# Optimization experiments

Hardware: AMD Instinct MI355X
Metric: run time of the kernel (lower is better)

Reference implementation:

```python
import jax, jax.numpy as jnp
import numpy as np

WIN = 8   # window size
NH = 6    # num heads
DIM = 192
PDIM = 256
S = 32    # D=H=W spatial extent


def window_partition(x, w):
    # x: (B, D, H, W, C) -> (nW, w**3, C)
    B, D, H, Wd, C = x.shape
    x = x.reshape(B, D // w, w, H // w, w, Wd // w, w, C)
    x = x.transpose(0, 1, 3, 5, 2, 4, 6, 7)
    return x.reshape(-1, w * w * w, C)


def window_reverse(win, w, B, D, H, Wd):
    C = win.shape[-1]
    x = win.reshape(B, D // w, H // w, Wd // w, w, w, w, C)
    x = x.transpose(0, 1, 4, 2, 5, 3, 6, 7)
    return x.reshape(B, D, H, Wd, C)


def layernorm(x, g, b, eps=1e-5):
    m = x.mean(-1, keepdims=True)
    v = ((x - m) ** 2).mean(-1, keepdims=True)
    return (x - m) / jnp.sqrt(v + eps) * g + b


def setup_inputs() -> dict:
    key = jax.random.key(0)
    ks = jax.random.split(key, 8)
    return {
        "x": jax.random.normal(ks[0], (1, DIM, S, S, S), jnp.float32),
        "prev_x": jax.random.normal(ks[1], (1, PDIM, S, S, S), jnp.float32),
        "fc1_w": jax.random.normal(ks[2], (PDIM, PDIM), jnp.float32) * 0.02,
        "fc1_b": jnp.zeros((PDIM,), jnp.float32),
        "fc2_w": jax.random.normal(ks[3], (DIM, PDIM), jnp.float32) * 0.02,
        "fc2_b": jnp.zeros((DIM,), jnp.float32),
        "q_w": jax.random.normal(ks[4], (DIM, DIM), jnp.float32) * 0.02,
        "q_b": jnp.zeros((DIM,), jnp.float32),
        "kv_w": jax.random.normal(ks[5], (2 * DIM, DIM), jnp.float32) * 0.02,
        "v_b": jnp.zeros((DIM,), jnp.float32),
        "proj_w": jax.random.normal(ks[6], (DIM, DIM), jnp.float32) * 0.02,
        "proj_b": jnp.zeros((DIM,), jnp.float32),
        "logit_scale": jnp.log(10.0) * jnp.ones((NH, 1, 1), jnp.float32),
        "ln_g": jnp.ones((DIM,), jnp.float32),
        "ln_b": jnp.zeros((DIM,), jnp.float32),
    }


def reference(x, prev_x, fc1_w, fc1_b, fc2_w, fc2_b, q_w, q_b, kv_w, v_b,
              proj_w, proj_b, logit_scale, ln_g, ln_b):
    B, C, D, H, Wd = x.shape
    xc = x.transpose(0, 2, 3, 4, 1)       # (B, D, H, W, C)
    pc = prev_x.transpose(0, 2, 3, 4, 1)   # (B, D, H, W, prev_dim)
    # mlp_match: Linear -> GELU(exact) -> Linear
    pc = jax.nn.gelu(pc @ fc1_w.T + fc1_b, approximate=False) @ fc2_w.T + fc2_b
    xw = window_partition(xc, WIN)         # (nW, N, C)
    pw = window_partition(pc, WIN)         # (nW, N, C)
    nW, N, _ = xw.shape
    hd = C // NH
    # q from x1, kv from x2 (k has no bias, v does)
    q = (xw @ q_w.T + q_b).reshape(nW, N, NH, hd).transpose(0, 2, 1, 3)
    kv_bias = jnp.concatenate([jnp.zeros_like(v_b), v_b])
    kv = (pw @ kv_w.T + kv_bias).reshape(nW, N, 2, NH, hd).transpose(2, 0, 3, 1, 4)
    k_, v_ = kv[0], kv[1]                  # (nW, H, N, hd)
    # cosine attention with clamped learned logit scale
    qn = q / jnp.maximum(jnp.linalg.norm(q, axis=-1, keepdims=True), 1e-12)
    kn = k_ / jnp.maximum(jnp.linalg.norm(k_, axis=-1, keepdims=True), 1e-12)
    scale = jnp.exp(jnp.minimum(logit_scale, jnp.log(1.0 / 0.01)))  # (H,1,1)
    attn = jnp.einsum('whnd,whmd->whnm', qn, kn) * scale
    attn = jax.nn.softmax(attn, axis=-1)
    out = jnp.einsum('whnm,whmd->whnd', attn, v_).transpose(0, 2, 1, 3).reshape(nW, N, C)
    out = out @ proj_w.T + proj_b
    xw = xw + layernorm(out, ln_g, ln_b)   # residual + cross_norm
    xr = window_reverse(xw, WIN, B, D, H, Wd)
    return xr.transpose(0, 4, 1, 2, 3)     # back to (B, C, D, H, W)
```

## Files before the change

### kernel.cpp

```cpp
#include <hip/hip_runtime.h>
#include <stdint.h>

typedef unsigned short u16;
typedef unsigned int u32;
typedef short short8 __attribute__((ext_vector_type(8)));
typedef float f32x4 __attribute__((ext_vector_type(4)));
typedef u32 u32x4 __attribute__((ext_vector_type(4)));

#define T_TOT 32768

__device__ __forceinline__ u16 f2bf(float f) {
  u32 u = __float_as_uint(f);
  return (u16)((u + 0x7fffu + ((u >> 16) & 1u)) >> 16);
}
__device__ __forceinline__ float bf2f(u16 h) {
  return __uint_as_float(((u32)h) << 16);
}
__device__ __forceinline__ u32 pk2(float a, float b) {
  return (u32)f2bf(a) | ((u32)f2bf(b) << 16);
}
__device__ __forceinline__ u32 cvtpk(float a, float b) {
  u32 r;
  asm("v_cvt_pk_bf16_f32 %0, %1, %2" : "=v"(r) : "v"(a), "v"(b));
  return r;
}

__device__ __forceinline__ void gld_lds16(const void* g, void* l) {
  __builtin_amdgcn_global_load_lds(
      (const __attribute__((address_space(1))) u32*)g,
      (__attribute__((address_space(3))) u32*)l, 16, 0, 0);
}

__device__ __forceinline__ void plswap(u32& a, u32& b) {
#if __has_builtin(__builtin_amdgcn_permlane32_swap) && \
    __has_builtin(__builtin_amdgcn_permlane16_swap)
  typedef u32 u32x2v __attribute__((ext_vector_type(2)));
  u32x2v r = __builtin_amdgcn_permlane32_swap(a, b, false, false);
  u32x2v w = __builtin_amdgcn_permlane16_swap(r[0], r[1], false, false);
  a = w[0]; b = w[1];
#else
  asm volatile(
      "s_nop 2\n\t"
      "v_permlane32_swap_b32 %0, %1\n\t"
      "s_nop 2\n\t"
      "v_permlane16_swap_b32 %0, %1\n\t"
      "s_nop 2"
      : "+v"(a), "+v"(b));
#endif
}

__global__ __launch_bounds__(256) void k_wconv(
    const float* __restrict__ fc1, const float* __restrict__ fc2,
    const float* __restrict__ qw, const float* __restrict__ kvw,
    const float* __restrict__ pw, u16* __restrict__ out) {
  int idx = blockIdx.x * 256 + threadIdx.x;
  const float* src; int K; int rel; u16* dst;
  if (idx < 8192)       { src = fc1; K = 256; rel = idx;         dst = out; }
  else if (idx < 14336) { src = fc2; K = 256; rel = idx - 8192;  dst = out + 65536; }
  else if (idx < 18944) { src = qw;  K = 192; rel = idx - 14336; dst = out + 114688; }
  else if (idx < 28160) { src = kvw; K = 192; rel = idx - 18944; dst = out + 151552; }
  else                  { src = pw;  K = 192; rel = idx - 28160; dst = out + 225280; }
  int nch = K >> 3;
  int m = rel / nch, ch = rel % nch;
  const float* sp = src + (size_t)m * K + ch * 8;
  int pos = (ch & ~7) | ((ch ^ m) & 7);
  u16* dp = dst + (size_t)m * K + pos * 8;
  ushort4 u0, u1;
  u0.x = f2bf(sp[0]); u0.y = f2bf(sp[1]); u0.z = f2bf(sp[2]); u0.w = f2bf(sp[3]);
  u1.x = f2bf(sp[4]); u1.y = f2bf(sp[5]); u1.z = f2bf(sp[6]); u1.w = f2bf(sp[7]);
  *(ushort4*)(dp) = u0;
  *(ushort4*)(dp + 4) = u1;
}

template<int C>
__global__ __launch_bounds__(256) void k_transpose(const float* __restrict__ src,
                                                   u16* __restrict__ dst) {
  __shared__ u16 sT[64][72];
  int c0 = blockIdx.x * 64, t0 = blockIdx.y * 64;
  int tid = threadIdx.x;
  for (int i = tid; i < 1024; i += 256) {
    int row = i >> 4;
    int tb  = (i & 15) * 4;
    const float* sp = src + (size_t)(c0 + row) * T_TOT + t0 + tb;
    float4 v = *(const float4*)sp;
    ushort4 u;
    u.x = f2bf(v.x); u.y = f2bf(v.y); u.z = f2bf(v.z); u.w = f2bf(v.w);
    *(ushort4*)(&sT[row][tb]) = u;
  }
  __syncthreads();
  int tl = tid & 63;
  int jb = tid >> 6;
  for (int p = 0; p < 2; ++p) {
    int j = jb + 4 * p;
    int t = t0 + tl;
    u16 e[8];
#pragma unroll
    for (int e8 = 0; e8 < 8; ++e8) e[e8] = sT[j * 8 + e8][tl];
    int pos = (c0 >> 3) + (j ^ (t & 7));
    uint4 o;
    o.x = (u32)e[0] | ((u32)e[1] << 16);
    o.y = (u32)e[2] | ((u32)e[3] << 16);
    o.z = (u32)e[4] | ((u32)e[5] << 16);
    o.w = (u32)e[6] | ((u32)e[7] << 16);
    *(uint4*)(dst + (size_t)t * C + pos * 8) = o;
  }
}

enum { EPI_FC1 = 0, EPI_FC2 = 1, EPI_Q = 2, EPI_KV = 3 };

template<int M, int K, int EPI>
__global__ __launch_bounds__(256) void k_gemm(const u16* __restrict__ W,
    const u16* __restrict__ B, const float* __restrict__ bias,
    const float* __restrict__ ls,
    u16* __restrict__ out, u16* __restrict__ out2) {
  __shared__ u16 lW[64 * 64];
  __shared__ u16 lB[128 * 64];
  int tid = threadIdx.x;
  int lane = tid & 63, wid = tid >> 6;
  int g = lane >> 4, c = lane & 15;
  int wm = wid >> 1, wt = wid & 1;
  int t0 = blockIdx.x * 128, m0 = blockIdx.y * 64;
  f32x4 acc[2][4];
#pragma unroll
  for (int i = 0; i < 2; ++i)
#pragma unroll
    for (int j = 0; j < 4; ++j) acc[i][j] = f32x4{0.f, 0.f, 0.f, 0.f};

  for (int s = 0; s < K / 64; ++s) {
    __syncthreads();
#pragma unroll
    for (int i0 = 0; i0 < 512; i0 += 256) {
      int i = i0 + tid;
      int r = i >> 3, ch = i & 7;
      gld_lds16(W + (size_t)(m0 + r) * K + s * 64 + ch * 8,
                lW + (size_t)(i & ~63) * 8);
    }
#pragma unroll
    for (int i0 = 0; i0 < 1024; i0 += 256) {
      int i = i0 + tid;
      int r = i >> 3, ch = i & 7;
      gld_lds16(B + (size_t)(t0 + r) * K + s * 64 + ch * 8,
                lB + (size_t)(i & ~63) * 8);
    }
    __syncthreads();
#pragma unroll
    for (int kc = 0; kc < 2; ++kc) {
      short8 af[2], bfr[4];
#pragma unroll
      for (int mt = 0; mt < 2; ++mt) {
        int r = wm * 32 + mt * 16 + c;
        af[mt] = *(const short8*)(lW + r * 64 + (((kc * 4 + g) ^ (r & 7)) << 3));
      }
#pragma unroll
      for (int tt = 0; tt < 4; ++tt) {
        int r = wt * 64 + tt * 16 + c;
        bfr[tt] = *(const short8*)(lB + r * 64 + (((kc * 4 + g) ^ (r & 7)) << 3));
      }
#pragma unroll
      for (int mt = 0; mt < 2; ++mt)
#pragma unroll
        for (int tt = 0; tt < 4; ++tt)
          acc[mt][tt] = __builtin_amdgcn_mfma_f32_16x16x32_bf16(
              af[mt], bfr[tt], acc[mt][tt], 0, 0, 0);
    }
  }

  float vv[2][4][4];
#pragma unroll
  for (int mt = 0; mt < 2; ++mt) {
    int m_base = m0 + wm * 32 + mt * 16 + 4 * g;
    float br[4];
    if constexpr (EPI == EPI_KV) {
      if (m_base < 192) { br[0] = br[1] = br[2] = br[3] = 0.f; }
      else {
        float4 b4 = *(const float4*)(bias + (m_base - 192));
        br[0] = b4.x; br[1] = b4.y; br[2] = b4.z; br[3] = b4.w;
      }
    } else {
      float4 b4 = *(const float4*)(bias + m_base);
      br[0] = b4.x; br[1] = b4.y; br[2] = b4.z; br[3] = b4.w;
    }
#pragma unroll
    for (int tt = 0; tt < 4; ++tt)
#pragma unroll
      for (int r = 0; r < 4; ++r) vv[mt][tt][r] = acc[mt][tt][r] + br[r];
  }

  if constexpr (EPI == EPI_Q || EPI == EPI_KV) {
    if (EPI == EPI_Q || m0 < 192) {
      float sc = 1.0f;
      if constexpr (EPI == EPI_Q) {
        int headq = (m0 + wm * 32) >> 5;
        sc = __expf(fminf(ls[headq], 4.6051701859880914f)) * 1.4426950408889634f;
      }
#pragma unroll
      for (int tt = 0; tt < 4; ++tt) {
        float ss = 0.f;
#pragma unroll
        for (int mt = 0; mt < 2; ++mt)
#pragma unroll
          for (int r = 0; r < 4; ++r) ss += vv[mt][tt][r] * vv[mt][tt][r];
        ss += __shfl_xor(ss, 16);
        ss += __shfl_xor(ss, 32);
        float rn = sc / fmaxf(sqrtf(ss), 1e-12f);
#pragma unroll
        for (int mt = 0; mt < 2; ++mt)
#pragma unroll
          for (int r = 0; r < 4; ++r) vv[mt][tt][r] *= rn;
      }
    }
  }

#pragma unroll
  for (int mt = 0; mt < 2; ++mt) {
    int m_base = m0 + wm * 32 + mt * 16 + 4 * g;
#pragma unroll
    for (int tt = 0; tt < 4; ++tt) {
      int t = t0 + wt * 64 + tt * 16 + c;
      float v[4];
#pragma unroll
      for (int r = 0; r < 4; ++r) v[r] = vv[mt][tt][r];
      if constexpr (EPI == EPI_FC1) {
#pragma unroll
        for (int r = 0; r < 4; ++r)
          v[r] = 0.5f * v[r] * (1.0f + erff(v[r] * 0.70710678118654752f));
      }
      if constexpr (EPI == EPI_FC1 || EPI == EPI_FC2) {
        ushort4 u;
        u.x = f2bf(v[0]); u.y = f2bf(v[1]); u.z = f2bf(v[2]); u.w = f2bf(v[3]);
        int pos = (m_base >> 3) ^ (t & 7);
        *(ushort4*)(out + (size_t)t * M + (pos << 3) + (m_base & 7)) = u;
      } else {
        int z = t >> 10, y = (t >> 5) & 31, xx = t & 31;
        int win = ((z >> 3) << 4) + ((y >> 3) << 2) + (xx >> 3);
        int n = ((z & 7) << 6) + ((y & 7) << 3) + (xx & 7);
        if (EPI == EPI_Q) {
          int head = m_base >> 5, dim = m_base & 31;
          ushort4 u;
          u.x = f2bf(v[0]); u.y = f2bf(v[1]); u.z = f2bf(v[2]); u.w = f2bf(v[3]);
          *(ushort4*)(out + ((size_t)(win * 6 + head) * 512 + n) * 32 + dim) = u;
        } else if (m_base < 192) {
          int head = m_base >> 5, dim = m_base & 31;
          ushort4 u;
          u.x = f2bf(v[0]); u.y = f2bf(v[1]); u.z = f2bf(v[2]); u.w = f2bf(v[3]);
          *(ushort4*)(out + ((size_t)(win * 6 + head) * 512 + n) * 36 + dim) = u;
        } else {
          int vb = m_base - 192;
          int head = vb >> 5, dimb = vb & 31;
#pragma unroll
          for (int r = 0; r < 4; ++r) {
            int dimr = dimb + r;
            out2[((size_t)(win * 6 + head) * 32 + dimr) * 512 +
                 (((n >> 3) ^ (dimr & 7)) << 3) + (n & 7)] = f2bf(v[r]);
          }
        }
      }
    }
  }
}

__global__ __launch_bounds__(256) void k_attn(const u16* __restrict__ Qw,
    const u16* __restrict__ Kw, const u16* __restrict__ Vw,
    u16* __restrict__ Amat) {
  __shared__ u16 Kn[512 * 36];
  int tid = threadIdx.x, lane = tid & 63, wid = tid >> 6;
  int g = lane >> 4, c = lane & 15;
  int zq = blockIdx.x / 6, head = blockIdx.x % 6, win = blockIdx.y;
  const u16* Kg = Kw + (size_t)(win * 6 + head) * 18432;
  const u16* Vg = Vw + (size_t)(win * 6 + head) * 16384;
  const u16* Qg = Qw + (size_t)(win * 6 + head) * 16384;
  for (int i = tid; i < 2304; i += 256)
    gld_lds16(Kg + (size_t)i * 8, Kn + (size_t)i * 8);
  __syncthreads();

  int wz = win >> 4, wy = (win >> 2) & 3, wx = win & 3;
  u32x4 onepk;
  onepk[0] = 0x3F803F80u; onepk[1] = 0x3F803F80u;
  onepk[2] = 0x3F803F80u; onepk[3] = 0x3F803F80u;
  short8 ONES = __builtin_bit_cast(short8, onepk);

  for (int qp = 0; qp < 2; ++qp) {
    int q0A = zq * 256 + wid * 64 + qp * 32;
    int q0B = q0A + 16;
    short8 qfA = *(const short8*)(Qg + (size_t)(q0A + c) * 32 + g * 8);
    short8 qfB = *(const short8*)(Qg + (size_t)(q0B + c) * 32 + g * 8);

    f32x4 o0A = {0.f, 0.f, 0.f, 0.f}, o1A = {0.f, 0.f, 0.f, 0.f};
    f32x4 o2A = {0.f, 0.f, 0.f, 0.f};
    f32x4 o0B = {0.f, 0.f, 0.f, 0.f}, o1B = {0.f, 0.f, 0.f, 0.f};
    f32x4 o2B = {0.f, 0.f, 0.f, 0.f};
#pragma unroll 4
    for (int cc = 0; cc < 16; ++cc) {
      short8 kf0 = *(const short8*)(Kn + (size_t)(cc * 32 + c) * 36 + g * 8);
      short8 kf1 = *(const short8*)(Kn + (size_t)(cc * 32 + 16 + c) * 36 + g * 8);
      int chpos = ((cc * 4 + g) ^ (c & 7)) << 3;
      short8 vf0 = *(const short8*)(Vg + (size_t)c * 512 + chpos);
      short8 vf1 = *(const short8*)(Vg + (size_t)(16 + c) * 512 + chpos);
      __builtin_amdgcn_s_setprio(1);
      f32x4 s0A = __builtin_amdgcn_mfma_f32_16x16x32_bf16(
          kf0, qfA, f32x4{0.f, 0.f, 0.f, 0.f}, 0, 0, 0);
      f32x4 s1A = __builtin_amdgcn_mfma_f32_16x16x32_bf16(
          kf1, qfA, f32x4{0.f, 0.f, 0.f, 0.f}, 0, 0, 0);
      f32x4 s0B = __builtin_amdgcn_mfma_f32_16x16x32_bf16(
          kf0, qfB, f32x4{0.f, 0.f, 0.f, 0.f}, 0, 0, 0);
      f32x4 s1B = __builtin_amdgcn_mfma_f32_16x16x32_bf16(
          kf1, qfB, f32x4{0.f, 0.f, 0.f, 0.f}, 0, 0, 0);
      __builtin_amdgcn_s_setprio(0);
      f32x4 p0A, p1A, p0B, p1B;
#pragma unroll
      for (int r = 0; r < 4; ++r) {
        p0A[r] = __builtin_amdgcn_exp2f(s0A[r]);
        p1A[r] = __builtin_amdgcn_exp2f(s1A[r]);
        p0B[r] = __builtin_amdgcn_exp2f(s0B[r]);
        p1B[r] = __builtin_amdgcn_exp2f(s1B[r]);
      }
      u32 waA = cvtpk(p0A[0], p0A[1]), wbA = cvtpk(p0A[2], p0A[3]);
      u32 wcA = cvtpk(p1A[0], p1A[1]), wdA = cvtpk(p1A[2], p1A[3]);
      plswap(waA, wcA);
      plswap(wbA, wdA);
      u32 waB = cvtpk(p0B[0], p0B[1]), wbB = cvtpk(p0B[2], p0B[3]);
      u32 wcB = cvtpk(p1B[0], p1B[1]), wdB = cvtpk(p1B[2], p1B[3]);
      plswap(waB, wcB);
      plswap(wbB, wdB);
      u32x4 pwA, pwB;
      pwA[0] = waA; pwA[1] = wbA; pwA[2] = wcA; pwA[3] = wdA;
      pwB[0] = waB; pwB[1] = wbB; pwB[2] = wcB; pwB[3] = wdB;
      short8 pfA = __builtin_bit_cast(short8, pwA);
      short8 pfB = __builtin_bit_cast(short8, pwB);
      __builtin_amdgcn_s_setprio(1);
      o0A = __builtin_amdgcn_mfma_f32_16x16x32_bf16(pfA, vf0, o0A, 0, 0, 0);
      o1A = __builtin_amdgcn_mfma_f32_16x16x32_bf16(pfA, vf1, o1A, 0, 0, 0);
      o2A = __builtin_amdgcn_mfma_f32_16x16x32_bf16(pfA, ONES, o2A, 0, 0, 0);
      o0B = __builtin_amdgcn_mfma_f32_16x16x32_bf16(pfB, vf0, o0B, 0, 0, 0);
      o1B = __builtin_amdgcn_mfma_f32_16x16x32_bf16(pfB, vf1, o1B, 0, 0, 0);
      o2B = __builtin_amdgcn_mfma_f32_16x16x32_bf16(pfB, ONES, o2B, 0, 0, 0);
      __builtin_amdgcn_s_setprio(0);
    }

#pragma unroll
    for (int half = 0; half < 2; ++half) {
      f32x4 oo0 = half ? o0B : o0A;
      f32x4 oo1 = half ? o1B : o1A;
      f32x4 osum = half ? o2B : o2A;
      int q0 = half ? q0B : q0A;
      int cg0 = head * 32 + c;
      int cg1 = cg0 + 16;
#pragma unroll
      for (int r = 0; r < 4; ++r) {
        float rs = 1.0f / osum[r];
        int n = q0 + 4 * g + r;
        int dz = n >> 6, dy = (n >> 3) & 7, dx = n & 7;
        int t = (wz * 8 + dz) * 1024 + (wy * 8 + dy) * 32 + wx * 8 + dx;
        Amat[(size_t)t * 192 + (((cg0 >> 3) ^ (t & 7)) << 3) + (cg0 & 7)] =
            f2bf(oo0[r] * rs);
        Amat[(size_t)t * 192 + (((cg1 >> 3) ^ (t & 7)) << 3) + (cg1 & 7)] =
            f2bf(oo1[r] * rs);
      }
    }
  }
}

__global__ __launch_bounds__(256) void k_proj_ln(const u16* __restrict__ W,
    const u16* __restrict__ B, const float* __restrict__ bias,
    const float* __restrict__ x, const float* __restrict__ gg,
    const float* __restrict__ bb, float* __restrict__ out) {
  __shared__ u16 lW[192 * 64];
  __shared__ u16 lB[64 * 64];
  __shared__ float red[2][4][64];
  int tid = threadIdx.x;
  int lane = tid & 63, wid = tid >> 6;
  int g = lane >> 4, c = lane & 15;
  int t0 = blockIdx.x * 64;
  f32x4 acc[3][4];
#pragma unroll
  for (int i = 0; i < 3; ++i)
#pragma unroll
    for (int j = 0; j < 4; ++j) acc[i][j] = f32x4{0.f, 0.f, 0.f, 0.f};

  for (int s = 0; s < 3; ++s) {
    __syncthreads();
#pragma unroll
    for (int i0 = 0; i0 < 1536; i0 += 256) {
      int i = i0 + tid;
      int r = i >> 3, ch = i & 7;
      gld_lds16(W + (size_t)r * 192 + s * 64 + ch * 8,
                lW + (size_t)(i & ~63) * 8);
    }
#pragma unroll
    for (int i0 = 0; i0 < 512; i0 += 256) {
      int ii = i0 + tid;
      int r = ii >> 3, ch = ii & 7;
      gld_lds16(B + (size_t)(t0 + r) * 192 + s * 64 + ch * 8,
                lB + (size_t)(ii & ~63) * 8);
    }
    __syncthreads();
#pragma unroll
    for (int kc = 0; kc < 2; ++kc) {
      short8 af[3], bfr[4];
#pragma unroll
      for (int mt = 0; mt < 3; ++mt) {
        int r = wid * 48 + mt * 16 + c;
        af[mt] = *(const short8*)(lW + r * 64 + (((kc * 4 + g) ^ (r & 7)) << 3));
      }
#pragma unroll
      for (int tt = 0; tt < 4; ++tt) {
        int r = tt * 16 + c;
        bfr[tt] = *(const short8*)(lB + r * 64 + (((kc * 4 + g) ^ (r & 7)) << 3));
      }
#pragma unroll
      for (int mt = 0; mt < 3; ++mt)
#pragma unroll
        for (int tt = 0; tt < 4; ++tt)
          acc[mt][tt] = __builtin_amdgcn_mfma_f32_16x16x32_bf16(
              af[mt], bfr[tt], acc[mt][tt], 0, 0, 0);
    }
  }

  float br[3][4];
#pragma unroll
  for (int mt = 0; mt < 3; ++mt) {
    float4 b4 = *(const float4*)(bias + wid * 48 + mt * 16 + 4 * g);
    br[mt][0] = b4.x; br[mt][1] = b4.y; br[mt][2] = b4.z; br[mt][3] = b4.w;
  }
  float s1[4], s2[4];
#pragma unroll
  for (int tt = 0; tt < 4; ++tt) {
    s1[tt] = 0.f; s2[tt] = 0.f;
#pragma unroll
    for (int mt = 0; mt < 3; ++mt)
#pragma unroll
      for (int r = 0; r < 4; ++r) {
        float v = acc[mt][tt][r] + br[mt][r];
        s1[tt] += v;
        s2[tt] += v * v;
      }
    s1[tt] += __shfl_xor(s1[tt], 16); s1[tt] += __shfl_xor(s1[tt], 32);
    s2[tt] += __shfl_xor(s2[tt], 16); s2[tt] += __shfl_xor(s2[tt], 32);
  }
  if (lane < 16) {
#pragma unroll
    for (int tt = 0; tt < 4; ++tt) {
      red[0][wid][tt * 16 + lane] = s1[tt];
      red[1][wid][tt * 16 + lane] = s2[tt];
    }
  }
  __syncthreads();
  float mean[4], rstd[4];
#pragma unroll
  for (int tt = 0; tt < 4; ++tt) {
    int tl = tt * 16 + c;
    float S1 = (red[0][0][tl] + red[0][1][tl]) + (red[0][2][tl] + red[0][3][tl]);
    float S2 = (red[1][0][tl] + red[1][1][tl]) + (red[1][2][tl] + red[1][3][tl]);
    float m = S1 * (1.0f / 192.0f);
    float var = S2 * (1.0f / 192.0f) - m * m;
    mean[tt] = m;
    rstd[tt] = rsqrtf(var + 1e-5f);
  }
#pragma unroll
  for (int mt = 0; mt < 3; ++mt) {
    int m_base = wid * 48 + mt * 16 + 4 * g;
#pragma unroll
    for (int r = 0; r < 4; ++r) {
      int ch = m_base + r;
      float ga = gg[ch], ba = bb[ch];
      const float* xp = x + (size_t)ch * T_TOT + t0;
      float* op = out + (size_t)ch * T_TOT + t0;
#pragma unroll
      for (int tt = 0; tt < 4; ++tt) {
        int tl = tt * 16 + c;
        float v = acc[mt][tt][r] + br[mt][r];
        op[tl] = xp[tl] + (v - mean[tt]) * rstd[tt] * ga + ba;
      }
    }
  }
}

extern "C" void kernel_launch(void* const* d_in, const int* in_sizes, int n_in,
                              void* d_out, int out_size, void* d_ws, size_t ws_size,
                              hipStream_t stream) {
  const float* x      = (const float*)d_in[0];
  const float* prev   = (const float*)d_in[1];
  const float* fc1_w  = (const float*)d_in[2];
  const float* fc1_b  = (const float*)d_in[3];
  const float* fc2_w  = (const float*)d_in[4];
  const float* fc2_b  = (const float*)d_in[5];
  const float* q_w    = (const float*)d_in[6];
  const float* q_b    = (const float*)d_in[7];
  const float* kv_w   = (const float*)d_in[8];
  const float* v_b    = (const float*)d_in[9];
  const float* proj_w = (const float*)d_in[10];
  const float* proj_b = (const float*)d_in[11];
  const float* lsc    = (const float*)d_in[12];
  const float* ln_g   = (const float*)d_in[13];
  const float* ln_b   = (const float*)d_in[14];
  float* out = (float*)d_out;
  char* ws = (char*)d_ws;

  u16* Pt   = (u16*)(ws + 0);
  u16* Y1t  = (u16*)(ws + 16777216);
  u16* Zt   = (u16*)(ws + 33554432);
  u16* Xt   = (u16*)(ws + 46137344);
  u16* Kwin = (u16*)(ws + 46137344);
  u16* Vwin = (u16*)(ws + 60293120);
  u16* Wbf  = (u16*)(ws + 72876032);
  u16* Qwin = Pt;
  u16* Amat = Y1t;

  k_wconv<<<128, 256, 0, stream>>>(fc1_w, fc2_w, q_w, kv_w, proj_w, Wbf);
  k_transpose<256><<<dim3(4, 512), 256, 0, stream>>>(prev, Pt);
  k_transpose<192><<<dim3(3, 512), 256, 0, stream>>>(x, Xt);
  k_gemm<256, 256, EPI_FC1><<<dim3(256, 4), 256, 0, stream>>>(Wbf, Pt, fc1_b, nullptr, Y1t, nullptr);
  k_gemm<192, 256, EPI_FC2><<<dim3(256, 3), 256, 0, stream>>>(Wbf + 65536, Y1t, fc2_b, nullptr, Zt, nullptr);
  k_gemm<192, 192, EPI_Q><<<dim3(256, 3), 256, 0, stream>>>(Wbf + 114688, Xt, q_b, lsc, Qwin, nullptr);
  k_gemm<384, 192, EPI_KV><<<dim3(256, 6), 256, 0, stream>>>(Wbf + 151552, Zt, v_b, nullptr, Kwin, Vwin);
  k_attn<<<dim3(12, 64), 256, 0, stream>>>(Qwin, Kwin, Vwin, Amat);
  k_proj_ln<<<512, 256, 0, stream>>>(Wbf + 225280, Amat, proj_b, x, ln_g, ln_b, out);
}
```

Measured before the change: 123.2 us.

## Load GEMM operands directly from global memory into registers, bypassing LDS

Both the generic GEMM and the proj+layernorm kernels stop staging W and B tiles in shared memory with barriers. Each wave now preloads its whole weight slice for the full K into registers and streams B fragments straight from global memory, using the same XOR swizzled index. This removes the LDS round trip and the __syncthreads, and may help occupancy through lower LDS use. In exchange it costs many more VGPRs (up to 16 short8 for K=256) and B rows are re-read by both the wm waves with no sharing through LDS.

Result: slower. 220.6 us (+79.1%).

```diff
diff --git a/kernel.cpp b/kernel.cpp
--- a/kernel.cpp
+++ b/kernel.cpp
@@ -15,9 +15,6 @@
 }
 __device__ __forceinline__ float bf2f(u16 h) {
   return __uint_as_float(((u32)h) << 16);
-}
-__device__ __forceinline__ u32 pk2(float a, float b) {
-  return (u32)f2bf(a) | ((u32)f2bf(b) << 16);
 }
 __device__ __forceinline__ u32 cvtpk(float a, float b) {
   u32 r;
@@ -113,56 +110,46 @@
     const u16* __restrict__ B, const float* __restrict__ bias,
     const float* __restrict__ ls,
     u16* __restrict__ out, u16* __restrict__ out2) {
-  __shared__ u16 lW[64 * 64];
-  __shared__ u16 lB[128 * 64];
+  constexpr int NKC = K / 32;
   int tid = threadIdx.x;
   int lane = tid & 63, wid = tid >> 6;
   int g = lane >> 4, c = lane & 15;
   int wm = wid >> 1, wt = wid & 1;
   int t0 = blockIdx.x * 128, m0 = blockIdx.y * 64;
+
+  short8 af[2][NKC];
+#pragma unroll
+  for (int mt = 0; mt < 2; ++mt) {
+    const u16* wr = W + (size_t)(m0 + wm * 32 + mt * 16 + c) * K;
+#pragma unroll
+    for (int kc = 0; kc < NKC; ++kc) {
+      int l = kc * 4 + g;
+      int pos = (l & ~7) | ((l ^ c) & 7);
+      af[mt][kc] = *(const short8*)(wr + pos * 8);
+    }
+  }
+  const u16* bt0 = B + (size_t)(t0 + wt * 64 + c) * K;
+
   f32x4 acc[2][4];
 #pragma unroll
   for (int i = 0; i < 2; ++i)
 #pragma unroll
     for (int j = 0; j < 4; ++j) acc[i][j] = f32x4{0.f, 0.f, 0.f, 0.f};
 
-  for (int s = 0; s < K / 64; ++s) {
-    __syncthreads();
-#pragma unroll
-    for (int i0 = 0; i0 < 512; i0 += 256) {
-      int i = i0 + tid;
-      int r = i >> 3, ch = i & 7;
-      gld_lds16(W + (size_t)(m0 + r) * K + s * 64 + ch * 8,
-                lW + (size_t)(i & ~63) * 8);
-    }
-#pragma unroll
-    for (int i0 = 0; i0 < 1024; i0 += 256) {
-      int i = i0 + tid;
-      int r = i >> 3, ch = i & 7;
-      gld_lds16(B + (size_t)(t0 + r) * K + s * 64 + ch * 8,
-                lB + (size_t)(i & ~63) * 8);
-    }
-    __syncthreads();
-#pragma unroll
-    for (int kc = 0; kc < 2; ++kc) {
-      short8 af[2], bfr[4];
-#pragma unroll
-      for (int mt = 0; mt < 2; ++mt) {
-        int r = wm * 32 + mt * 16 + c;
-        af[mt] = *(const short8*)(lW + r * 64 + (((kc * 4 + g) ^ (r & 7)) << 3));
-      }
-#pragma unroll
-      for (int tt = 0; tt < 4; ++tt) {
-        int r = wt * 64 + tt * 16 + c;
-        bfr[tt] = *(const short8*)(lB + r * 64 + (((kc * 4 + g) ^ (r & 7)) << 3));
-      }
-#pragma unroll
-      for (int mt = 0; mt < 2; ++mt)
-#pragma unroll
-        for (int tt = 0; tt < 4; ++tt)
-          acc[mt][tt] = __builtin_amdgcn_mfma_f32_16x16x32_bf16(
-              af[mt], bfr[tt], acc[mt][tt], 0, 0, 0);
-    }
+#pragma unroll 2
+  for (int kc = 0; kc < NKC; ++kc) {
+    int l = kc * 4 + g;
+    int pos8 = ((l & ~7) | ((l ^ c) & 7)) * 8;
+    short8 bfr[4];
+#pragma unroll
+    for (int tt = 0; tt < 4; ++tt)
+      bfr[tt] = *(const short8*)(bt0 + (size_t)(tt * 16) * K + pos8);
+#pragma unroll
+    for (int mt = 0; mt < 2; ++mt)
+#pragma unroll
+      for (int tt = 0; tt < 4; ++tt)
+        acc[mt][tt] = __builtin_amdgcn_mfma_f32_16x16x32_bf16(
+            af[mt][kc], bfr[tt], acc[mt][tt], 0, 0, 0);
   }
 
   float vv[2][4][4];
@@ -364,56 +351,45 @@
     const u16* __restrict__ B, const float* __restrict__ bias,
     const float* __restrict__ x, const float* __restrict__ gg,
     const float* __restrict__ bb, float* __restrict__ out) {
-  __shared__ u16 lW[192 * 64];
-  __shared__ u16 lB[64 * 64];
   __shared__ float red[2][4][64];
   int tid = threadIdx.x;
   int lane = tid & 63, wid = tid >> 6;
   int g = lane >> 4, c = lane & 15;
   int t0 = blockIdx.x * 64;
+
+  short8 af[3][6];
+#pragma unroll
+  for (int mt = 0; mt < 3; ++mt) {
+    const u16* wr = W + (size_t)(wid * 48 + mt * 16 + c) * 192;
+#pragma unroll
+    for (int kc = 0; kc < 6; ++kc) {
+      int l = kc * 4 + g;
+      int pos = (l & ~7) | ((l ^ c) & 7);
+      af[mt][kc] = *(const short8*)(wr + pos * 8);
+    }
+  }
+  const u16* bt0 = B + (size_t)(t0 + c) * 192;
+
   f32x4 acc[3][4];
 #pragma unroll
   for (int i = 0; i < 3; ++i)
 #pragma unroll
     for (int j = 0; j < 4; ++j) acc[i][j] = f32x4{0.f, 0.f, 0.f, 0.f};
 
-  for (int s = 0; s < 3; ++s) {
-    __syncthreads();
-#pragma unroll
-    for (int i0 = 0; i0 < 1536; i0 += 256) {
-      int i = i0 + tid;
-      int r = i >> 3, ch = i & 7;
-      gld_lds16(W + (size_t)r * 192 + s * 64 + ch * 8,
-                lW + (size_t)(i & ~63) * 8);
-    }
-#pragma unroll
-    for (int i0 = 0; i0 < 512; i0 += 256) {
-      int ii = i0 + tid;
-      int r = ii >> 3, ch = ii & 7;
-      gld_lds16(B + (size_t)(t0 + r) * 192 + s * 64 + ch * 8,
-                lB + (size_t)(ii & ~63) * 8);
-    }
-    __syncthreads();
-#pragma unroll
-    for (int kc = 0; kc < 2; ++kc) {
-      short8 af[3], bfr[4];
-#pragma unroll
-      for (int mt = 0; mt < 3; ++mt) {
-        int r = wid * 48 + mt * 16 + c;
-        af[mt] = *(const short8*)(lW + r * 64 + (((kc * 4 + g) ^ (r & 7)) << 3));
-      }
-#pragma unroll
-      for (int tt = 0; tt < 4; ++tt) {
-        int r = tt * 16 + c;
-        bfr[tt] = *(const short8*)(lB + r * 64 + (((kc * 4 + g) ^ (r & 7)) << 3));
-      }
-#pragma unroll
-      for (int mt = 0; mt < 3; ++mt)
-#pragma unroll
-        for (int tt = 0; tt < 4; ++tt)
-          acc[mt][tt] = __builtin_amdgcn_mfma_f32_16x16x32_bf16(
-              af[mt], bfr[tt], acc[mt][tt], 0, 0, 0);
-    }
+#pragma unroll 2
+  for (int kc = 0; kc < 6; ++kc) {
+    int l = kc * 4 + g;
+    int pos8 = ((l & ~7) | ((l ^ c) & 7)) * 8;
+    short8 bfr[4];
+#pragma unroll
+    for (int tt = 0; tt < 4; ++tt)
+      bfr[tt] = *(const short8*)(bt0 + (size_t)(tt * 16) * 192 + pos8);
+#pragma unroll
+    for (int mt = 0; mt < 3; ++mt)
+#pragma unroll
+      for (int tt = 0; tt < 4; ++tt)
+        acc[mt][tt] = __builtin_amdgcn_mfma_f32_16x16x32_bf16(
+            af[mt][kc], bfr[tt], acc[mt][tt], 0, 0, 0);
   }
 
   float br[3][4];
```
